# Optimization experiments

Measured on AMD Instinct MI355X. Metric: run time of the kernel, lower is better.

Reference implementation:

```python
import jax, jax.numpy as jnp
import numpy as np

B, N_IMG, D = 256, 128, 768
E, S, H = 3, 44, 1024  # S = ceil(128/3) rounded up to multiple of 4; H = 4*D//E
MAX_SLOTS = 88
LN_EPS = 1e-5


def setup_inputs() -> dict:
    key = jax.random.key(0)
    ks = jax.random.split(key, 12)
    x = jax.random.normal(ks[0], (B, N_IMG + 1, D), dtype=jnp.float32)
    attn_weight = jax.random.uniform(ks[1], (B, N_IMG), dtype=jnp.float32)
    ln_gamma = jnp.ones((D,), jnp.float32)
    ln_beta = jnp.zeros((D,), jnp.float32)
    vsg_w = jax.random.normal(ks[2], (D + 1, D), jnp.float32) / np.sqrt(D + 1)
    vsg_b = jnp.zeros((D,), jnp.float32)
    mu = jax.random.normal(ks[3], (E, D, MAX_SLOTS), jnp.float32) / np.sqrt(D)
    scale = jnp.ones((1,), jnp.float32)
    # per-expert MLP: kaiming-ish / xavier-ish random params
    w1 = jax.random.normal(ks[4], (E, D, H), jnp.float32) * np.sqrt(2.0 / D)
    b1 = jnp.zeros((E, H), jnp.float32)
    w2 = jax.random.normal(ks[5], (E, H, D), jnp.float32) * np.sqrt(2.0 / (H + D))
    b2 = jnp.zeros((E, D), jnp.float32)
    cw1 = jax.random.normal(ks[6], (D, 4 * D), jnp.float32) * np.sqrt(2.0 / D)
    cb1 = jnp.zeros((4 * D,), jnp.float32)
    cw2 = jax.random.normal(ks[7], (4 * D, D), jnp.float32) * np.sqrt(2.0 / (4 * D))
    cb2 = jnp.zeros((D,), jnp.float32)
    return dict(x=x, attn_weight=attn_weight, ln_gamma=ln_gamma, ln_beta=ln_beta,
                vsg_w=vsg_w, vsg_b=vsg_b, mu=mu, scale=scale,
                w1=w1, b1=b1, w2=w2, b2=b2, cw1=cw1, cb1=cb1, cw2=cw2, cb2=cb2)


def reference(x, attn_weight, ln_gamma, ln_beta, vsg_w, vsg_b, mu, scale,
              w1, b1, w2, b2, cw1, cb1, cw2, cb2):
    b, np1, d = x.shape
    n = np1 - 1
    img = x[:, 1:, :]            # [B, N, D]
    cls = x[:, 0, :]             # [B, D]

    # LayerNorm on image tokens
    mean = img.mean(-1, keepdims=True)
    var = img.var(-1, keepdims=True)  # biased, matches torch LayerNorm
    img_n = (img - mean) * jax.lax.rsqrt(var + LN_EPS) * ln_gamma + ln_beta

    # slot bias from [cls_feat, mean attention] -> visible_slot_gen (mode='original')
    attn_feat = attn_weight.mean(axis=1, keepdims=True)            # [B, 1]
    slot_input = jnp.concatenate([cls, attn_feat], axis=-1)        # [B, D+1]
    slot_bias = slot_input @ vsg_w + vsg_b                         # [B, D]

    # adjusted slot prototypes: mu[:, :, :S].permute(1,0,2) + slot_bias broadcast over (E, S)
    adj_mu = mu[:, :, :S].transpose(1, 0, 2)[None] + slot_bias[:, :, None, None]  # [B, D, E, S]

    logits = jnp.einsum('bnd,bdes->bnes', img_n * scale, adj_mu)   # [B, N, E, S]

    # expert group mask from attention thresholds (groups (1,1,1))
    vis = attn_weight > 0.7
    part = (attn_weight >= 0.3) & (attn_weight <= 0.7)
    occ = attn_weight < 0.3
    emask = jnp.stack([vis, part, occ], axis=-1).astype(logits.dtype)  # [B, N, E]
    logits = logits * emask[:, :, :, None]

    # softmax over tokens (dispatch) and over flattened slots (combine)
    dispatch = jax.nn.softmax(logits, axis=1)                      # [B, N, E, S]
    combine = jax.nn.softmax(logits.reshape(b, n, E * S), axis=-1) # [B, N, E*S]

    slot_in = jnp.einsum('bnd,bnes->besd', img, dispatch)          # [B, E, S, D]

    # batched per-expert MLP (fused grouped GEMM instead of python loop)
    h = jax.nn.gelu(jnp.einsum('besd,edh->besh', slot_in, w1) + b1[:, None, :],
                    approximate=False)
    slot_out = jnp.einsum('besh,ehd->besd', h, w2) + b2[:, None, :]  # [B, E, S, D]

    slot_flat = slot_out.reshape(b, E * S, d)
    img_out = jnp.einsum('bsd,bns->bnd', slot_flat, combine)       # [B, N, D]

    # CLS token through its dedicated dense MLP
    cls_h = jax.nn.gelu(cls @ cw1 + cb1, approximate=False)
    cls_out = cls_h @ cw2 + cb2                                    # [B, D]

    return jnp.concatenate([cls_out[:, None, :], img_out], axis=1)  # [B, N+1, D]
```

## Files before the change

kernel.cpp:

```cpp
#include <hip/hip_runtime.h>
#include <hip/hip_bf16.h>
#include <math.h>

#define NB   256
#define NIMG 128
#define DIM  768
#define NE   3
#define NS   44
#define NH   1024
#define ESL  132
#define NTOK (NB*NIMG)
#define MAXSLOTS 88
#define BIGI (1 << 30)

typedef __bf16 bf16x8 __attribute__((ext_vector_type(8)));
typedef float f32x4 __attribute__((ext_vector_type(4)));
typedef unsigned short us8 __attribute__((ext_vector_type(8)));

__device__ __forceinline__ float gelu_f(float v) {
    return 0.5f * v * (1.0f + erff(v * 0.70710678118654752f));
}

__device__ __forceinline__ float block_reduce_sum256(float v, float* red) {
    int tid = threadIdx.x;
    red[tid] = v;
    __syncthreads();
    for (int s = 128; s > 0; s >>= 1) {
        if (tid < s) red[tid] += red[tid + s];
        __syncthreads();
    }
    float r = red[0];
    __syncthreads();
    return r;
}

__global__ void repack_mu_k(const float* __restrict__ mu, __hip_bfloat16* __restrict__ bt) {
    int idx = blockIdx.x * 256 + threadIdx.x;
    if (idx >= 256 * DIM) return;
    int r = idx / DIM, d = idx - r * DIM;
    float v = 0.f;
    if (r < ESL) {
        int e = r / NS, s = r - e * NS;
        v = mu[((size_t)e * DIM + d) * MAXSLOTS + s];
    }
    bt[idx] = __float2bfloat16(v);
}

__global__ void transpose_bf16_k(const float* __restrict__ in, __hip_bfloat16* __restrict__ outp,
                                 int R, int Cc) {
    __shared__ float t[32][33];
    in   += (size_t)blockIdx.z * R * Cc;
    outp += (size_t)blockIdx.z * R * Cc;
    int c0 = blockIdx.x * 32, r0 = blockIdx.y * 32;
    int tx = threadIdx.x, ty = threadIdx.y;
    for (int i = 0; i < 32; i += 8) {
        int r = r0 + ty + i, c = c0 + tx;
        t[ty + i][tx] = (r < R && c < Cc) ? in[(size_t)r * Cc + c] : 0.f;
    }
    __syncthreads();
    for (int i = 0; i < 32; i += 8) {
        int r = c0 + ty + i, c = r0 + tx;
        if (r < Cc && c < R) outp[(size_t)r * R + c] = __float2bfloat16(t[tx][ty + i]);
    }
}

__global__ void cls_bf16_k(const float* __restrict__ x, __hip_bfloat16* __restrict__ cls16) {
    int idx = blockIdx.x * 256 + threadIdx.x;
    if (idx >= NB * DIM) return;
    int b = idx / DIM, j = idx - b * DIM;
    cls16[idx] = __float2bfloat16(x[(size_t)b * 129 * DIM + j]);
}

__global__ void slot_bias_k(const float* __restrict__ x, const float* __restrict__ aw,
                            const float* __restrict__ vsg_w, const float* __restrict__ vsg_b,
                            float* __restrict__ slot_bias) {
    __shared__ float red[256];
    __shared__ float cls[DIM];
    int b = blockIdx.x, tid = threadIdx.x;
    float a = (tid < NIMG) ? aw[b * NIMG + tid] : 0.f;
    float af = block_reduce_sum256(a, red) * (1.0f / NIMG);
    for (int j = tid; j < DIM; j += 256) cls[j] = x[(size_t)b * 129 * DIM + j];
    __syncthreads();
    int j0 = tid, j1 = tid + 256, j2 = tid + 512;
    float acc0 = 0.f, acc1 = 0.f, acc2 = 0.f;
    for (int d = 0; d < DIM; ++d) {
        float c = cls[d];
        const float* wr = vsg_w + (size_t)d * DIM;
        acc0 = fmaf(c, wr[j0], acc0);
        acc1 = fmaf(c, wr[j1], acc1);
        acc2 = fmaf(c, wr[j2], acc2);
    }
    const float* wl = vsg_w + (size_t)DIM * DIM;
    float* out = slot_bias + (size_t)b * DIM;
    out[j0] = acc0 + vsg_b[j0] + af * wl[j0];
    out[j1] = acc1 + vsg_b[j1] + af * wl[j1];
    out[j2] = acc2 + vsg_b[j2] + af * wl[j2];
}

__global__ void ln_t2_k(const float* __restrict__ x, const float* __restrict__ gamma,
                        const float* __restrict__ beta, const float* __restrict__ slot_bias,
                        __hip_bfloat16* __restrict__ img_n, float* __restrict__ t2) {
    __shared__ float red[256];
    int tok = blockIdx.x;
    int b = tok >> 7, n = tok & 127;
    int tid = threadIdx.x;
    const float* row = x + ((size_t)b * 129 + 1 + n) * DIM;
    float v0 = row[tid], v1 = row[tid + 256], v2 = row[tid + 512];
    float s  = block_reduce_sum256(v0 + v1 + v2, red);
    float ss = block_reduce_sum256(v0*v0 + v1*v1 + v2*v2, red);
    float mean = s * (1.0f / DIM);
    float var  = ss * (1.0f / DIM) - mean * mean;
    float inv  = rsqrtf(var + 1e-5f);
    const float* sb = slot_bias + (size_t)b * DIM;
    __hip_bfloat16* orow = img_n + (size_t)tok * DIM;
    float tacc = 0.f;
    int j = tid;
    float y0 = (v0 - mean) * inv * gamma[j] + beta[j]; orow[j] = __float2bfloat16(y0); tacc = fmaf(y0, sb[j], tacc);
    j = tid + 256;
    float y1 = (v1 - mean) * inv * gamma[j] + beta[j]; orow[j] = __float2bfloat16(y1); tacc = fmaf(y1, sb[j], tacc);
    j = tid + 512;
    float y2 = (v2 - mean) * inv * gamma[j] + beta[j]; orow[j] = __float2bfloat16(y2); tacc = fmaf(y2, sb[j], tacc);
    float t = block_reduce_sum256(tacc, red);
    if (tid == 0) t2[tok] = t;
}

__global__ void mask_k(float* __restrict__ L, const float* __restrict__ t2,
                       const float* __restrict__ aw, const float* __restrict__ scale) {
    int idx = blockIdx.x * 256 + threadIdx.x;
    if (idx >= NTOK * ESL) return;
    int tok = idx / ESL, r = idx - tok * ESL;
    int e = r / NS;
    float a = aw[tok];
    int sel = (a > 0.7f) ? 0 : ((a >= 0.3f) ? 1 : 2);
    float v = 0.f;
    if (e == sel) v = scale[0] * (L[idx] + t2[tok]);
    L[idx] = v;
}

__global__ void dispatch_k(const float* __restrict__ L, float* __restrict__ dT) {
    __shared__ float red[128];
    int es = blockIdx.x, b = blockIdx.y, tid = threadIdx.x;
    float v = L[((size_t)(b * NIMG + tid)) * ESL + es];
    red[tid] = v; __syncthreads();
    for (int s = 64; s > 0; s >>= 1) { if (tid < s) red[tid] = fmaxf(red[tid], red[tid + s]); __syncthreads(); }
    float mx = red[0]; __syncthreads();
    float e = __expf(v - mx);
    red[tid] = e; __syncthreads();
    for (int s = 64; s > 0; s >>= 1) { if (tid < s) red[tid] += red[tid + s]; __syncthreads(); }
    float sum = red[0];
    dT[((size_t)b * ESL + es) * NIMG + tid] = e / sum;
}

__global__ void combine_k(const float* __restrict__ L, float* __restrict__ C) {
    int tok = blockIdx.x, lane = threadIdx.x;
    const float* row = L + (size_t)tok * ESL;
    float v0 = row[lane], v1 = row[lane + 64];
    bool has2 = lane < (ESL - 128);
    float v2 = has2 ? row[lane + 128] : -1e30f;
    float m = fmaxf(fmaxf(v0, v1), v2);
    for (int o = 32; o > 0; o >>= 1) m = fmaxf(m, __shfl_xor(m, o));
    float e0 = __expf(v0 - m), e1 = __expf(v1 - m);
    float e2 = has2 ? __expf(v2 - m) : 0.f;
    float s = e0 + e1 + e2;
    for (int o = 32; o > 0; o >>= 1) s += __shfl_xor(s, o);
    float inv = 1.0f / s;
    float* orow = C + (size_t)tok * ESL;
    orow[lane] = e0 * inv;
    orow[lane + 64] = e1 * inv;
    if (has2) orow[lane + 128] = e2 * inv;
}

#define LDSS 40

__global__ __launch_bounds__(256)
void mfma_gemm_k(const __hip_bfloat16* __restrict__ A_, long long aBS, int lda,
                 const __hip_bfloat16* __restrict__ Bt_, long long bBS, int ldb,
                 const float* __restrict__ bias, long long biasBS,
                 void* __restrict__ Cv, long long cBS, int ldc, int cSub, int cOuter,
                 int Nlim, int K, int act, int out_bf16)
{
    const unsigned short* A  = (const unsigned short*)A_  + (long long)blockIdx.z * aBS;
    const unsigned short* Bt = (const unsigned short*)Bt_ + (long long)blockIdx.z * bBS;
    if (bias) bias += (long long)blockIdx.z * biasBS;
    long long cbase = (long long)blockIdx.z * cBS;

    __shared__ unsigned short As[128 * LDSS];
    __shared__ unsigned short Bs[128 * LDSS];

    int tid = threadIdx.x;
    int m0 = blockIdx.y * 128, n0 = blockIdx.x * 128;

    int srow = tid >> 2, sk = (tid & 3) * 8;
    const unsigned short* gA = A  + (long long)(m0 + srow) * lda + sk;
    const unsigned short* gB = Bt + (long long)(n0 + srow) * ldb + sk;
    int lofs  = srow * LDSS + sk;
    int lofs2 = (srow + 64) * LDSS + sk;

    int lane = tid & 63, wv = tid >> 6;
    int wm = (wv >> 1) * 64, wn = (wv & 1) * 64;
    int lrow = lane & 15, quad = lane >> 4;

    int a_off[4], b_off[4];
#pragma unroll
    for (int i = 0; i < 4; ++i) {
        a_off[i] = (wm + i * 16 + lrow) * LDSS + quad * 8;
        b_off[i] = (wn + i * 16 + lrow) * LDSS + quad * 8;
    }

    f32x4 acc[4][4] = {};

    for (int k0 = 0; k0 < K; k0 += 32) {
        us8 a0 = *(const us8*)(gA + k0);
        us8 a1 = *(const us8*)(gA + (long long)64 * lda + k0);
        us8 b0 = *(const us8*)(gB + k0);
        us8 b1 = *(const us8*)(gB + (long long)64 * ldb + k0);
        __syncthreads();
        *(us8*)(As + lofs)  = a0;
        *(us8*)(As + lofs2) = a1;
        *(us8*)(Bs + lofs)  = b0;
        *(us8*)(Bs + lofs2) = b1;
        __syncthreads();
        bf16x8 af[4], bfr[4];
#pragma unroll
        for (int i = 0; i < 4; ++i) {
            af[i]  = *(const bf16x8*)(As + a_off[i]);
            bfr[i] = *(const bf16x8*)(Bs + b_off[i]);
        }
#pragma unroll
        for (int i = 0; i < 4; ++i)
#pragma unroll
            for (int j = 0; j < 4; ++j)
                acc[i][j] = __builtin_amdgcn_mfma_f32_16x16x32_bf16(af[i], bfr[j], acc[i][j], 0, 0, 0);
    }

    float* Cf = (float*)Cv;
    __hip_bfloat16* Cb = (__hip_bfloat16*)Cv;
#pragma unroll
    for (int mi = 0; mi < 4; ++mi) {
#pragma unroll
        for (int r = 0; r < 4; ++r) {
            int row = m0 + wm + mi * 16 + quad * 4 + r;
            int q = row / cSub;
            long long rbase = cbase + (long long)(q * cOuter + (row - q * cSub)) * ldc;
#pragma unroll
            for (int ni = 0; ni < 4; ++ni) {
                int col = n0 + wn + ni * 16 + lrow;
                if (col < Nlim) {
                    float v = acc[mi][ni][r];
                    if (bias) v += bias[col];
                    if (act == 1) v = gelu_f(v);
                    if (out_bf16) Cb[rbase + col] = __float2bfloat16(v);
                    else          Cf[rbase + col] = v;
                }
            }
        }
    }
}

#define GTM 64
#define GTN 64
#define GTK 16

__global__ __launch_bounds__(256)
void gemm_k(const float* __restrict__ A, long long aBS, int lda, int aSub, int aOuter,
            const float* __restrict__ W, long long wBS, int ldw,
            const float* __restrict__ bias, long long biasBS,
            void* __restrict__ Cv, long long cBS, int ldc, int cSub, int cOuter,
            int M, int N, int K, int act, int out_bf16) {
    A += (long long)blockIdx.z * aBS;
    W += (long long)blockIdx.z * wBS;
    if (bias != nullptr) bias += (long long)blockIdx.z * biasBS;
    long long cbase = (long long)blockIdx.z * cBS;

    __shared__ float As[GTK][GTM + 4];
    __shared__ float Ws[GTK][GTN];

    int tid = threadIdx.x;
    int tx = tid & 15, ty = tid >> 4;
    int m0 = blockIdx.y * GTM, n0 = blockIdx.x * GTN;

    int am = tid >> 2, akq = tid & 3;
    int arow_g = m0 + am;
    bool arow_ok = arow_g < M;
    int aq = arow_g / aSub;
    long long aoff = (long long)(aq * aOuter + (arow_g - aq * aSub)) * lda;

    int wn = tid & 63, wg = tid >> 6;
    bool wcol_ok = (n0 + wn) < N;

    float acc[4][4] = {{0.f}};

    for (int k0 = 0; k0 < K; k0 += GTK) {
        float4 av = make_float4(0.f, 0.f, 0.f, 0.f);
        int ak = k0 + akq * 4;
        if (arow_ok && ak < K) av = *(const float4*)(A + aoff + ak);
        As[akq * 4 + 0][am] = av.x;
        As[akq * 4 + 1][am] = av.y;
        As[akq * 4 + 2][am] = av.z;
        As[akq * 4 + 3][am] = av.w;
#pragma unroll
        for (int jj = 0; jj < 4; ++jj) {
            int kk = wg * 4 + jj;
            float wv = 0.f;
            if (wcol_ok && (k0 + kk) < K) wv = W[(long long)(k0 + kk) * ldw + n0 + wn];
            Ws[kk][wn] = wv;
        }
        __syncthreads();
#pragma unroll
        for (int kk = 0; kk < GTK; ++kk) {
            const float4 a4 = *(const float4*)(&As[kk][ty * 4]);
            const float4 w4 = *(const float4*)(&Ws[kk][tx * 4]);
            float a[4] = {a4.x, a4.y, a4.z, a4.w};
            float w[4] = {w4.x, w4.y, w4.z, w4.w};
#pragma unroll
            for (int i = 0; i < 4; ++i)
#pragma unroll
                for (int jq = 0; jq < 4; ++jq)
                    acc[i][jq] = fmaf(a[i], w[jq], acc[i][jq]);
        }
        __syncthreads();
    }

    int col = n0 + tx * 4;
    bool col_ok = col < N;
    float4 bv = make_float4(0.f, 0.f, 0.f, 0.f);
    if (bias != nullptr && col_ok) bv = *(const float4*)(bias + col);
    float* Cf = (float*)Cv;
    __hip_bfloat16* Cb = (__hip_bfloat16*)Cv;
#pragma unroll
    for (int i = 0; i < 4; ++i) {
        int row = m0 + ty * 4 + i;
        if (row < M && col_ok) {
            int q = row / cSub;
            long long coff = cbase + (long long)(q * cOuter + (row - q * cSub)) * ldc + col;
            float4 v = make_float4(acc[i][0] + bv.x, acc[i][1] + bv.y,
                                   acc[i][2] + bv.z, acc[i][3] + bv.w);
            if (act == 1) { v.x = gelu_f(v.x); v.y = gelu_f(v.y); v.z = gelu_f(v.z); v.w = gelu_f(v.w); }
            if (out_bf16) {
                Cb[coff + 0] = __float2bfloat16(v.x);
                Cb[coff + 1] = __float2bfloat16(v.y);
                Cb[coff + 2] = __float2bfloat16(v.z);
                Cb[coff + 3] = __float2bfloat16(v.w);
            } else {
                *(float4*)(Cf + coff) = v;
            }
        }
    }
}

static inline void launch_gemm(hipStream_t st,
                               const float* A, long long aBS, int lda, int aSub, int aOuter,
                               const float* W, long long wBS, int ldw,
                               const float* bias, long long biasBS,
                               void* C, long long cBS, int ldc, int cSub, int cOuter,
                               int M, int N, int K, int act, int batch, int out_bf16) {
    dim3 grid((N + GTN - 1) / GTN, (M + GTM - 1) / GTM, batch);
    gemm_k<<<grid, dim3(256), 0, st>>>(A, aBS, lda, aSub, aOuter, W, wBS, ldw,
                                       bias, biasBS, C, cBS, ldc, cSub, cOuter, M, N, K, act, out_bf16);
}

extern "C" void kernel_launch(void* const* d_in, const int* in_sizes, int n_in,
                              void* d_out, int out_size, void* d_ws, size_t ws_size,
                              hipStream_t stream) {
    const float* x     = (const float*)d_in[0];
    const float* aw    = (const float*)d_in[1];
    const float* gamma = (const float*)d_in[2];
    const float* beta  = (const float*)d_in[3];
    const float* vsg_w = (const float*)d_in[4];
    const float* vsg_b = (const float*)d_in[5];
    const float* mu    = (const float*)d_in[6];
    const float* scale = (const float*)d_in[7];
    const float* w1    = (const float*)d_in[8];
    const float* b1    = (const float*)d_in[9];
    const float* w2    = (const float*)d_in[10];
    const float* b2    = (const float*)d_in[11];
    const float* cw1   = (const float*)d_in[12];
    const float* cb1   = (const float*)d_in[13];
    const float* cw2   = (const float*)d_in[14];
    const float* cb2   = (const float*)d_in[15];
    float* out = (float*)d_out;

    float* ws = (float*)d_ws;

    const long long IMGN_FL = (long long)NTOK * DIM / 2;
    const long long LOG_FL  = (long long)NTOK * ESL;
    __hip_bfloat16* img_n = (__hip_bfloat16*)ws;
    float* logits = ws + IMGN_FL;
    float* dT     = ws + IMGN_FL + LOG_FL;
    __hip_bfloat16* h = (__hip_bfloat16*)ws;
    long long o = IMGN_FL + 2 * LOG_FL;
    float* comb = ws + o;                   o += LOG_FL;
    __hip_bfloat16* slot_in = (__hip_bfloat16*)(ws + o); o += (long long)NE * NB * NS * DIM / 2;
    float* slot_out = ws + o;               o += (long long)NB * ESL * DIM;
    __hip_bfloat16* mu_p  = (__hip_bfloat16*)(ws + o); o += 256 * DIM / 2;
    float* slot_bias = ws + o;              o += NB * DIM;
    float* t2        = ws + o;              o += NTOK;
    __hip_bfloat16* w1t  = (__hip_bfloat16*)(ws + o); o += (long long)NE * NH * DIM / 2;
    __hip_bfloat16* w2t  = (__hip_bfloat16*)(ws + o); o += (long long)NE * DIM * NH / 2;
    __hip_bfloat16* cw1t = (__hip_bfloat16*)(ws + o); o += (long long)4 * DIM * DIM / 2;
    __hip_bfloat16* cw2t = (__hip_bfloat16*)(ws + o); o += (long long)4 * DIM * DIM / 2;
    __hip_bfloat16* cls16 = (__hip_bfloat16*)(ws + o); o += NB * DIM / 2;
    __hip_bfloat16* cls_h = (__hip_bfloat16*)(ws + o); o += (long long)NB * 4 * DIM / 2;

    repack_mu_k<<<(256 * DIM + 255) / 256, 256, 0, stream>>>(mu, mu_p);
    transpose_bf16_k<<<dim3(NH / 32, DIM / 32, NE), dim3(32, 8), 0, stream>>>(w1, w1t, DIM, NH);
    transpose_bf16_k<<<dim3(DIM / 32, NH / 32, NE), dim3(32, 8), 0, stream>>>(w2, w2t, NH, DIM);
    transpose_bf16_k<<<dim3(4 * DIM / 32, DIM / 32, 1), dim3(32, 8), 0, stream>>>(cw1, cw1t, DIM, 4 * DIM);
    transpose_bf16_k<<<dim3(DIM / 32, 4 * DIM / 32, 1), dim3(32, 8), 0, stream>>>(cw2, cw2t, 4 * DIM, DIM);
    cls_bf16_k<<<(NB * DIM + 255) / 256, 256, 0, stream>>>(x, cls16);

    slot_bias_k<<<NB, 256, 0, stream>>>(x, aw, vsg_w, vsg_b, slot_bias);
    ln_t2_k<<<NTOK, 256, 0, stream>>>(x, gamma, beta, slot_bias, img_n, t2);

    mfma_gemm_k<<<dim3(2, NTOK / 128, 1), 256, 0, stream>>>(
        img_n, 0, DIM, mu_p, 0, DIM, nullptr, 0,
        logits, 0, ESL, BIGI, 0, ESL, DIM, 0, 0);

    mask_k<<<(NTOK * ESL + 255) / 256, 256, 0, stream>>>(logits, t2, aw, scale);
    dispatch_k<<<dim3(ESL, NB), 128, 0, stream>>>(logits, dT);
    combine_k<<<NTOK, 64, 0, stream>>>(logits, comb);

    launch_gemm(stream, dT, (long long)ESL * NIMG, NIMG, BIGI, 0,
                x + DIM, (long long)129 * DIM, DIM, nullptr, 0,
                slot_in, (long long)NS * DIM, DIM, NS, NB * NS,
                ESL, DIM, NIMG, 0, NB, 1);

    mfma_gemm_k<<<dim3(NH / 128, NB * NS / 128, NE), 256, 0, stream>>>(
        slot_in, (long long)NB * NS * DIM, DIM,
        w1t, (long long)NH * DIM, DIM, b1, NH,
        h, (long long)NB * NS * NH, NH, BIGI, 0, NH, DIM, 1, 1);

    mfma_gemm_k<<<dim3(DIM / 128, NB * NS / 128, NE), 256, 0, stream>>>(
        h, (long long)NB * NS * NH, NH,
        w2t, (long long)DIM * NH, NH, b2, DIM,
        slot_out, (long long)NS * DIM, DIM, NS, ESL, DIM, NH, 0, 0);

    launch_gemm(stream, comb, (long long)NIMG * ESL, ESL, BIGI, 0,
                slot_out, (long long)ESL * DIM, DIM, nullptr, 0,
                out + DIM, (long long)129 * DIM, DIM, BIGI, 0,
                NIMG, DIM, ESL, 0, NB, 0);

    mfma_gemm_k<<<dim3(4 * DIM / 128, NB / 128, 1), 256, 0, stream>>>(
        cls16, 0, DIM, cw1t, 0, DIM, cb1, 0,
        cls_h, 0, 4 * DIM, BIGI, 0, 4 * DIM, DIM, 1, 1);
    mfma_gemm_k<<<dim3(DIM / 128, NB / 128, 1), 256, 0, stream>>>(
        cls_h, 0, 4 * DIM, cw2t, 0, 4 * DIM, cb2, 0,
        out, 0, DIM, 1, 129, DIM, 4 * DIM, 0, 0);
}
```

Before: 1.077 ms.

## Move dispatch and combine GEMMs to bf16 MFMA with direct-to-LDS loads

The two fp32 SIMT GEMMs (dispatch-weighted token aggregation and combine-weighted slot scatter) are replaced by the bf16 MFMA kernel. To feed it, the dispatch and combine weights are written as bf16, the image tokens are transposed into a bf16 buffer, and the second expert GEMM writes its output transposed with K padded to 160. The MFMA kernel now stages tiles with global_load_lds into an XOR-swizzled LDS layout in place of register staging with padding, and clamps out-of-range rows. This adds a transpose pass over x, lowers the precision of the routing weights and the image input, and the zero padding of slot_outT's extra K columns is not obviously guaranteed.

```diff
diff --git a/kernel.cpp b/kernel.cpp
--- a/kernel.cpp
+++ b/kernel.cpp
@@ -12,10 +12,12 @@
 #define NTOK (NB*NIMG)
 #define MAXSLOTS 88
 #define BIGI (1 << 30)
+#define KPAD 160
 
 typedef __bf16 bf16x8 __attribute__((ext_vector_type(8)));
 typedef float f32x4 __attribute__((ext_vector_type(4)));
-typedef unsigned short us8 __attribute__((ext_vector_type(8)));
+typedef const __attribute__((address_space(1))) void* gas_t;
+typedef __attribute__((address_space(3))) void* las_t;
 
 __device__ __forceinline__ float gelu_f(float v) {
     return 0.5f * v * (1.0f + erff(v * 0.70710678118654752f));
@@ -47,10 +49,10 @@
 }
 
 __global__ void transpose_bf16_k(const float* __restrict__ in, __hip_bfloat16* __restrict__ outp,
-                                 int R, int Cc) {
+                                 int R, int Cc, long long inBS, long long outBS) {
     __shared__ float t[32][33];
-    in   += (size_t)blockIdx.z * R * Cc;
-    outp += (size_t)blockIdx.z * R * Cc;
+    in   += (long long)blockIdx.z * inBS;
+    outp += (long long)blockIdx.z * outBS;
     int c0 = blockIdx.x * 32, r0 = blockIdx.y * 32;
     int tx = threadIdx.x, ty = threadIdx.y;
     for (int i = 0; i < 32; i += 8) {
@@ -137,7 +139,7 @@
     L[idx] = v;
 }
 
-__global__ void dispatch_k(const float* __restrict__ L, float* __restrict__ dT) {
+__global__ void dispatch_k(const float* __restrict__ L, __hip_bfloat16* __restrict__ dT16) {
     __shared__ float red[128];
     int es = blockIdx.x, b = blockIdx.y, tid = threadIdx.x;
     float v = L[((size_t)(b * NIMG + tid)) * ESL + es];
@@ -148,10 +150,10 @@
     red[tid] = e; __syncthreads();
     for (int s = 64; s > 0; s >>= 1) { if (tid < s) red[tid] += red[tid + s]; __syncthreads(); }
     float sum = red[0];
-    dT[((size_t)b * ESL + es) * NIMG + tid] = e / sum;
-}
-
-__global__ void combine_k(const float* __restrict__ L, float* __restrict__ C) {
+    dT16[((size_t)b * ESL + es) * NIMG + tid] = __float2bfloat16(e / sum);
+}
+
+__global__ void combine_k(const float* __restrict__ L, __hip_bfloat16* __restrict__ C) {
     int tok = blockIdx.x, lane = threadIdx.x;
     const float* row = L + (size_t)tok * ESL;
     float v0 = row[lane], v1 = row[lane + 64];
@@ -164,67 +166,74 @@
     float s = e0 + e1 + e2;
     for (int o = 32; o > 0; o >>= 1) s += __shfl_xor(s, o);
     float inv = 1.0f / s;
-    float* orow = C + (size_t)tok * ESL;
-    orow[lane] = e0 * inv;
-    orow[lane + 64] = e1 * inv;
-    if (has2) orow[lane + 128] = e2 * inv;
-}
-
-#define LDSS 40
+    __hip_bfloat16* orow = C + (size_t)tok * KPAD;
+    orow[lane] = __float2bfloat16(e0 * inv);
+    orow[lane + 64] = __float2bfloat16(e1 * inv);
+    if (has2) orow[lane + 128] = __float2bfloat16(e2 * inv);
+    else if (lane < KPAD - 128) orow[lane + 128] = __float2bfloat16(0.f);
+}
 
 __global__ __launch_bounds__(256)
-void mfma_gemm_k(const __hip_bfloat16* __restrict__ A_, long long aBS, int lda,
-                 const __hip_bfloat16* __restrict__ Bt_, long long bBS, int ldb,
-                 const float* __restrict__ bias, long long biasBS,
-                 void* __restrict__ Cv, long long cBS, int ldc, int cSub, int cOuter,
-                 int Nlim, int K, int act, int out_bf16)
+void mfma2_k(const __hip_bfloat16* __restrict__ A_, long long aBS, int lda, int Mrows,
+             const __hip_bfloat16* __restrict__ Bt_, long long bBS, int ldb, int Nrows,
+             const float* __restrict__ bias, long long biasBS,
+             void* __restrict__ Cv, long long cBS, int ldc, int cSub, long long cOuter,
+             int Mlim, int Nlim, int K, int act, int out_bf16, int ctrans)
 {
     const unsigned short* A  = (const unsigned short*)A_  + (long long)blockIdx.z * aBS;
     const unsigned short* Bt = (const unsigned short*)Bt_ + (long long)blockIdx.z * bBS;
     if (bias) bias += (long long)blockIdx.z * biasBS;
     long long cbase = (long long)blockIdx.z * cBS;
 
-    __shared__ unsigned short As[128 * LDSS];
-    __shared__ unsigned short Bs[128 * LDSS];
+    __shared__ unsigned short As[128 * 32];
+    __shared__ unsigned short Bs[128 * 32];
 
     int tid = threadIdx.x;
+    int lane = tid & 63, wv = tid >> 6;
     int m0 = blockIdx.y * 128, n0 = blockIdx.x * 128;
 
-    int srow = tid >> 2, sk = (tid & 3) * 8;
-    const unsigned short* gA = A  + (long long)(m0 + srow) * lda + sk;
-    const unsigned short* gB = Bt + (long long)(n0 + srow) * ldb + sk;
-    int lofs  = srow * LDSS + sk;
-    int lofs2 = (srow + 64) * LDSS + sk;
-
-    int lane = tid & 63, wv = tid >> 6;
+    const unsigned short* ga[2];
+    const unsigned short* gb[2];
+    int ldsoff[2];
+#pragma unroll
+    for (int i = 0; i < 2; ++i) {
+        int j = wv * 2 + i;
+        int p = j * 64 + lane;
+        int r = p >> 2;
+        int cg = (p & 3) ^ ((r >> 1) & 3);
+        int ra = m0 + r; if (ra > Mrows - 1) ra = Mrows - 1;
+        int rb = n0 + r; if (rb > Nrows - 1) rb = Nrows - 1;
+        ga[i] = A  + (long long)ra * lda + cg * 8;
+        gb[i] = Bt + (long long)rb * ldb + cg * 8;
+        ldsoff[i] = j * 512;
+    }
+
+    int lrow = lane & 15, quad = lane >> 4;
     int wm = (wv >> 1) * 64, wn = (wv & 1) * 64;
-    int lrow = lane & 15, quad = lane >> 4;
-
-    int a_off[4], b_off[4];
+    int offA[4], offB[4];
 #pragma unroll
     for (int i = 0; i < 4; ++i) {
-        a_off[i] = (wm + i * 16 + lrow) * LDSS + quad * 8;
-        b_off[i] = (wn + i * 16 + lrow) * LDSS + quad * 8;
+        int rowa = wm + i * 16 + lrow;
+        offA[i] = rowa * 32 + ((quad ^ ((rowa >> 1) & 3)) * 8);
+        int rowb = wn + i * 16 + lrow;
+        offB[i] = rowb * 32 + ((quad ^ ((rowb >> 1) & 3)) * 8);
     }
 
     f32x4 acc[4][4] = {};
 
     for (int k0 = 0; k0 < K; k0 += 32) {
-        us8 a0 = *(const us8*)(gA + k0);
-        us8 a1 = *(const us8*)(gA + (long long)64 * lda + k0);
-        us8 b0 = *(const us8*)(gB + k0);
-        us8 b1 = *(const us8*)(gB + (long long)64 * ldb + k0);
         __syncthreads();
-        *(us8*)(As + lofs)  = a0;
-        *(us8*)(As + lofs2) = a1;
-        *(us8*)(Bs + lofs)  = b0;
-        *(us8*)(Bs + lofs2) = b1;
+#pragma unroll
+        for (int i = 0; i < 2; ++i) {
+            __builtin_amdgcn_global_load_lds((gas_t)(ga[i] + k0), (las_t)(As + ldsoff[i]), 16, 0, 0);
+            __builtin_amdgcn_global_load_lds((gas_t)(gb[i] + k0), (las_t)(Bs + ldsoff[i]), 16, 0, 0);
+        }
         __syncthreads();
         bf16x8 af[4], bfr[4];
 #pragma unroll
         for (int i = 0; i < 4; ++i) {
-            af[i]  = *(const bf16x8*)(As + a_off[i]);
-            bfr[i] = *(const bf16x8*)(Bs + b_off[i]);
+            af[i]  = *(const bf16x8*)(As + offA[i]);
+            bfr[i] = *(const bf16x8*)(Bs + offB[i]);
         }
 #pragma unroll
         for (int i = 0; i < 4; ++i)
@@ -240,8 +249,11 @@
 #pragma unroll
         for (int r = 0; r < 4; ++r) {
             int row = m0 + wm + mi * 16 + quad * 4 + r;
+            if (row >= Mlim) continue;
             int q = row / cSub;
-            long long rbase = cbase + (long long)(q * cOuter + (row - q * cSub)) * ldc;
+            int sl = row - q * cSub;
+            long long rb = ctrans ? (cbase + (long long)q * cOuter + sl)
+                                  : (cbase + ((long long)q * cOuter + sl) * ldc);
 #pragma unroll
             for (int ni = 0; ni < 4; ++ni) {
                 int col = n0 + wn + ni * 16 + lrow;
@@ -249,114 +261,25 @@
                     float v = acc[mi][ni][r];
                     if (bias) v += bias[col];
                     if (act == 1) v = gelu_f(v);
-                    if (out_bf16) Cb[rbase + col] = __float2bfloat16(v);
-                    else          Cf[rbase + col] = v;
+                    long long off = ctrans ? (rb + (long long)col * ldc) : (rb + col);
+                    if (out_bf16) Cb[off] = __float2bfloat16(v);
+                    else          Cf[off] = v;
                 }
             }
         }
     }
 }
 
-#define GTM 64
-#define GTN 64
-#define GTK 16
-
-__global__ __launch_bounds__(256)
-void gemm_k(const float* __restrict__ A, long long aBS, int lda, int aSub, int aOuter,
-            const float* __restrict__ W, long long wBS, int ldw,
-            const float* __restrict__ bias, long long biasBS,
-            void* __restrict__ Cv, long long cBS, int ldc, int cSub, int cOuter,
-            int M, int N, int K, int act, int out_bf16) {
-    A += (long long)blockIdx.z * aBS;
-    W += (long long)blockIdx.z * wBS;
-    if (bias != nullptr) bias += (long long)blockIdx.z * biasBS;
-    long long cbase = (long long)blockIdx.z * cBS;
-
-    __shared__ float As[GTK][GTM + 4];
-    __shared__ float Ws[GTK][GTN];
-
-    int tid = threadIdx.x;
-    int tx = tid & 15, ty = tid >> 4;
-    int m0 = blockIdx.y * GTM, n0 = blockIdx.x * GTN;
-
-    int am = tid >> 2, akq = tid & 3;
-    int arow_g = m0 + am;
-    bool arow_ok = arow_g < M;
-    int aq = arow_g / aSub;
-    long long aoff = (long long)(aq * aOuter + (arow_g - aq * aSub)) * lda;
-
-    int wn = tid & 63, wg = tid >> 6;
-    bool wcol_ok = (n0 + wn) < N;
-
-    float acc[4][4] = {{0.f}};
-
-    for (int k0 = 0; k0 < K; k0 += GTK) {
-        float4 av = make_float4(0.f, 0.f, 0.f, 0.f);
-        int ak = k0 + akq * 4;
-        if (arow_ok && ak < K) av = *(const float4*)(A + aoff + ak);
-        As[akq * 4 + 0][am] = av.x;
-        As[akq * 4 + 1][am] = av.y;
-        As[akq * 4 + 2][am] = av.z;
-        As[akq * 4 + 3][am] = av.w;
-#pragma unroll
-        for (int jj = 0; jj < 4; ++jj) {
-            int kk = wg * 4 + jj;
-            float wv = 0.f;
-            if (wcol_ok && (k0 + kk) < K) wv = W[(long long)(k0 + kk) * ldw + n0 + wn];
-            Ws[kk][wn] = wv;
-        }
-        __syncthreads();
-#pragma unroll
-        for (int kk = 0; kk < GTK; ++kk) {
-            const float4 a4 = *(const float4*)(&As[kk][ty * 4]);
-            const float4 w4 = *(const float4*)(&Ws[kk][tx * 4]);
-            float a[4] = {a4.x, a4.y, a4.z, a4.w};
-            float w[4] = {w4.x, w4.y, w4.z, w4.w};
-#pragma unroll
-            for (int i = 0; i < 4; ++i)
-#pragma unroll
-                for (int jq = 0; jq < 4; ++jq)
-                    acc[i][jq] = fmaf(a[i], w[jq], acc[i][jq]);
-        }
-        __syncthreads();
-    }
-
-    int col = n0 + tx * 4;
-    bool col_ok = col < N;
-    float4 bv = make_float4(0.f, 0.f, 0.f, 0.f);
-    if (bias != nullptr && col_ok) bv = *(const float4*)(bias + col);
-    float* Cf = (float*)Cv;
-    __hip_bfloat16* Cb = (__hip_bfloat16*)Cv;
-#pragma unroll
-    for (int i = 0; i < 4; ++i) {
-        int row = m0 + ty * 4 + i;
-        if (row < M && col_ok) {
-            int q = row / cSub;
-            long long coff = cbase + (long long)(q * cOuter + (row - q * cSub)) * ldc + col;
-            float4 v = make_float4(acc[i][0] + bv.x, acc[i][1] + bv.y,
-                                   acc[i][2] + bv.z, acc[i][3] + bv.w);
-            if (act == 1) { v.x = gelu_f(v.x); v.y = gelu_f(v.y); v.z = gelu_f(v.z); v.w = gelu_f(v.w); }
-            if (out_bf16) {
-                Cb[coff + 0] = __float2bfloat16(v.x);
-                Cb[coff + 1] = __float2bfloat16(v.y);
-                Cb[coff + 2] = __float2bfloat16(v.z);
-                Cb[coff + 3] = __float2bfloat16(v.w);
-            } else {
-                *(float4*)(Cf + coff) = v;
-            }
-        }
-    }
-}
-
-static inline void launch_gemm(hipStream_t st,
-                               const float* A, long long aBS, int lda, int aSub, int aOuter,
-                               const float* W, long long wBS, int ldw,
-                               const float* bias, long long biasBS,
-                               void* C, long long cBS, int ldc, int cSub, int cOuter,
-                               int M, int N, int K, int act, int batch, int out_bf16) {
-    dim3 grid((N + GTN - 1) / GTN, (M + GTM - 1) / GTM, batch);
-    gemm_k<<<grid, dim3(256), 0, st>>>(A, aBS, lda, aSub, aOuter, W, wBS, ldw,
-                                       bias, biasBS, C, cBS, ldc, cSub, cOuter, M, N, K, act, out_bf16);
+static inline void mfma2(hipStream_t st, dim3 grid,
+                         const void* A, long long aBS, int lda, int Mrows,
+                         const void* Bt, long long bBS, int ldb, int Nrows,
+                         const float* bias, long long biasBS,
+                         void* C, long long cBS, int ldc, int cSub, long long cOuter,
+                         int Mlim, int Nlim, int K, int act, int obf, int ct) {
+    mfma2_k<<<grid, dim3(256), 0, st>>>((const __hip_bfloat16*)A, aBS, lda, Mrows,
+                                        (const __hip_bfloat16*)Bt, bBS, ldb, Nrows,
+                                        bias, biasBS, C, cBS, ldc, cSub, cOuter,
+                                        Mlim, Nlim, K, act, obf, ct);
 }
 
 extern "C" void kernel_launch(void* const* d_in, const int* in_sizes, int n_in,
@@ -384,66 +307,73 @@
 
     const long long IMGN_FL = (long long)NTOK * DIM / 2;
     const long long LOG_FL  = (long long)NTOK * ESL;
+    const long long REG1_FL = (long long)NE * NB * NS * NH / 2;
     __hip_bfloat16* img_n = (__hip_bfloat16*)ws;
     float* logits = ws + IMGN_FL;
-    float* dT     = ws + IMGN_FL + LOG_FL;
     __hip_bfloat16* h = (__hip_bfloat16*)ws;
-    long long o = IMGN_FL + 2 * LOG_FL;
-    float* comb = ws + o;                   o += LOG_FL;
+    long long o = REG1_FL;
+    __hip_bfloat16* dT16    = (__hip_bfloat16*)(ws + o); o += (long long)NB * ESL * NIMG / 2;
+    __hip_bfloat16* comb_p  = (__hip_bfloat16*)(ws + o); o += (long long)NTOK * KPAD / 2;
+    __hip_bfloat16* imgT    = (__hip_bfloat16*)(ws + o);
+    __hip_bfloat16* slot_outT = imgT;                    o += (long long)NB * DIM * KPAD / 2;
     __hip_bfloat16* slot_in = (__hip_bfloat16*)(ws + o); o += (long long)NE * NB * NS * DIM / 2;
-    float* slot_out = ws + o;               o += (long long)NB * ESL * DIM;
-    __hip_bfloat16* mu_p  = (__hip_bfloat16*)(ws + o); o += 256 * DIM / 2;
-    float* slot_bias = ws + o;              o += NB * DIM;
-    float* t2        = ws + o;              o += NTOK;
-    __hip_bfloat16* w1t  = (__hip_bfloat16*)(ws + o); o += (long long)NE * NH * DIM / 2;
-    __hip_bfloat16* w2t  = (__hip_bfloat16*)(ws + o); o += (long long)NE * DIM * NH / 2;
-    __hip_bfloat16* cw1t = (__hip_bfloat16*)(ws + o); o += (long long)4 * DIM * DIM / 2;
-    __hip_bfloat16* cw2t = (__hip_bfloat16*)(ws + o); o += (long long)4 * DIM * DIM / 2;
-    __hip_bfloat16* cls16 = (__hip_bfloat16*)(ws + o); o += NB * DIM / 2;
-    __hip_bfloat16* cls_h = (__hip_bfloat16*)(ws + o); o += (long long)NB * 4 * DIM / 2;
+    __hip_bfloat16* mu_p    = (__hip_bfloat16*)(ws + o); o += 256 * DIM / 2;
+    float* slot_bias = ws + o;                           o += NB * DIM;
+    float* t2        = ws + o;                           o += NTOK;
+    __hip_bfloat16* w1t  = (__hip_bfloat16*)(ws + o);    o += (long long)NE * NH * DIM / 2;
+    __hip_bfloat16* w2t  = (__hip_bfloat16*)(ws + o);    o += (long long)NE * DIM * NH / 2;
+    __hip_bfloat16* cw1t = (__hip_bfloat16*)(ws + o);    o += (long long)4 * DIM * DIM / 2;
+    __hip_bfloat16* cw2t = (__hip_bfloat16*)(ws + o);    o += (long long)4 * DIM * DIM / 2;
+    __hip_bfloat16* cls16 = (__hip_bfloat16*)(ws + o);   o += NB * DIM / 2;
+    __hip_bfloat16* cls_h = (__hip_bfloat16*)(ws + o);   o += (long long)NB * 4 * DIM / 2;
 
     repack_mu_k<<<(256 * DIM + 255) / 256, 256, 0, stream>>>(mu, mu_p);
-    transpose_bf16_k<<<dim3(NH / 32, DIM / 32, NE), dim3(32, 8), 0, stream>>>(w1, w1t, DIM, NH);
-    transpose_bf16_k<<<dim3(DIM / 32, NH / 32, NE), dim3(32, 8), 0, stream>>>(w2, w2t, NH, DIM);
-    transpose_bf16_k<<<dim3(4 * DIM / 32, DIM / 32, 1), dim3(32, 8), 0, stream>>>(cw1, cw1t, DIM, 4 * DIM);
-    transpose_bf16_k<<<dim3(DIM / 32, 4 * DIM / 32, 1), dim3(32, 8), 0, stream>>>(cw2, cw2t, 4 * DIM, DIM);
+    transpose_bf16_k<<<dim3(NH / 32, DIM / 32, NE), dim3(32, 8), 0, stream>>>(w1, w1t, DIM, NH, (long long)DIM * NH, (long long)NH * DIM);
+    transpose_bf16_k<<<dim3(DIM / 32, NH / 32, NE), dim3(32, 8), 0, stream>>>(w2, w2t, NH, DIM, (long long)NH * DIM, (long long)DIM * NH);
+    transpose_bf16_k<<<dim3(4 * DIM / 32, DIM / 32, 1), dim3(32, 8), 0, stream>>>(cw1, cw1t, DIM, 4 * DIM, 0, 0);
+    transpose_bf16_k<<<dim3(DIM / 32, 4 * DIM / 32, 1), dim3(32, 8), 0, stream>>>(cw2, cw2t, 4 * DIM, DIM, 0, 0);
     cls_bf16_k<<<(NB * DIM + 255) / 256, 256, 0, stream>>>(x, cls16);
+    transpose_bf16_k<<<dim3(DIM / 32, NIMG / 32, NB), dim3(32, 8), 0, stream>>>(x + DIM, imgT, NIMG, DIM, (long long)129 * DIM, (long long)DIM * NIMG);
 
     slot_bias_k<<<NB, 256, 0, stream>>>(x, aw, vsg_w, vsg_b, slot_bias);
     ln_t2_k<<<NTOK, 256, 0, stream>>>(x, gamma, beta, slot_bias, img_n, t2);
 
-    mfma_gemm_k<<<dim3(2, NTOK / 128, 1), 256, 0, stream>>>(
-        img_n, 0, DIM, mu_p, 0, DIM, nullptr, 0,
-        logits, 0, ESL, BIGI, 0, ESL, DIM, 0, 0);
+    mfma2(stream, dim3(2, NTOK / 128, 1),
+          img_n, 0, DIM, NTOK, mu_p, 0, DIM, 256, nullptr, 0,
+          logits, 0, ESL, BIGI, 0, NTOK, ESL, DIM, 0, 0, 0);
 
     mask_k<<<(NTOK * ESL + 255) / 256, 256, 0, stream>>>(logits, t2, aw, scale);
-    dispatch_k<<<dim3(ESL, NB), 128, 0, stream>>>(logits, dT);
-    combine_k<<<NTOK, 64, 0, stream>>>(logits, comb);
-
-    launch_gemm(stream, dT, (long long)ESL * NIMG, NIMG, BIGI, 0,
-                x + DIM, (long long)129 * DIM, DIM, nullptr, 0,
-                slot_in, (long long)NS * DIM, DIM, NS, NB * NS,
-                ESL, DIM, NIMG, 0, NB, 1);
-
-    mfma_gemm_k<<<dim3(NH / 128, NB * NS / 128, NE), 256, 0, stream>>>(
-        slot_in, (long long)NB * NS * DIM, DIM,
-        w1t, (long long)NH * DIM, DIM, b1, NH,
-        h, (long long)NB * NS * NH, NH, BIGI, 0, NH, DIM, 1, 1);
-
-    mfma_gemm_k<<<dim3(DIM / 128, NB * NS / 128, NE), 256, 0, stream>>>(
-        h, (long long)NB * NS * NH, NH,
-        w2t, (long long)DIM * NH, NH, b2, DIM,
-        slot_out, (long long)NS * DIM, DIM, NS, ESL, DIM, NH, 0, 0);
-
-    launch_gemm(stream, comb, (long long)NIMG * ESL, ESL, BIGI, 0,
-                slot_out, (long long)ESL * DIM, DIM, nullptr, 0,
-                out + DIM, (long long)129 * DIM, DIM, BIGI, 0,
-                NIMG, DIM, ESL, 0, NB, 0);
-
-    mfma_gemm_k<<<dim3(4 * DIM / 128, NB / 128, 1), 256, 0, stream>>>(
-        cls16, 0, DIM, cw1t, 0, DIM, cb1, 0,
-        cls_h, 0, 4 * DIM, BIGI, 0, 4 * DIM, DIM, 1, 1);
-    mfma_gemm_k<<<dim3(DIM / 128, NB / 128, 1), 256, 0, stream>>>(
-        cls_h, 0, 4 * DIM, cw2t, 0, 4 * DIM, cb2, 0,
-        out, 0, DIM, 1, 129, DIM, 4 * DIM, 0, 0);
-}
+    dispatch_k<<<dim3(ESL, NB), 128, 0, stream>>>(logits, dT16);
+    combine_k<<<NTOK, 64, 0, stream>>>(logits, comb_p);
+
+    mfma2(stream, dim3(DIM / 128, 2, NB),
+          dT16, (long long)ESL * NIMG, NIMG, ESL,
+          imgT, (long long)DIM * NIMG, NIMG, DIM, nullptr, 0,
+          slot_in, (long long)NS * DIM, DIM, NS, NB * NS,
+          ESL, DIM, NIMG, 0, 1, 0);
+
+    mfma2(stream, dim3(NH / 128, NB * NS / 128, NE),
+          slot_in, (long long)NB * NS * DIM, DIM, NB * NS,
+          w1t, (long long)NH * DIM, DIM, NH, b1, NH,
+          h, (long long)NB * NS * NH, NH, BIGI, 0,
+          NB * NS, NH, DIM, 1, 1, 0);
+
+    mfma2(stream, dim3(DIM / 128, NB * NS / 128, NE),
+          h, (long long)NB * NS * NH, NH, NB * NS,
+          w2t, (long long)DIM * NH, NH, DIM, b2, DIM,
+          slot_outT, NS, KPAD, NS, (long long)DIM * KPAD,
+          NB * NS, DIM, NH, 0, 1, 1);
+
+    mfma2(stream, dim3(DIM / 128, 1, NB),
+          comb_p, (long long)NIMG * KPAD, KPAD, NIMG,
+          slot_outT, (long long)DIM * KPAD, KPAD, DIM, nullptr, 0,
+          out + DIM, (long long)129 * DIM, DIM, BIGI, 0,
+          NIMG, DIM, KPAD, 0, 0, 0);
+
+    mfma2(stream, dim3(4 * DIM / 128, NB / 128, 1),
+          cls16, 0, DIM, NB, cw1t, 0, DIM, 4 * DIM, cb1, 0,
+          cls_h, 0, 4 * DIM, BIGI, 0, NB, 4 * DIM, DIM, 1, 1, 0);
+    mfma2(stream, dim3(DIM / 128, NB / 128, 1),
+          cls_h, 0, 4 * DIM, NB, cw2t, 0, 4 * DIM, DIM, cb2, 0,
+          out, 0, DIM, 1, 129, NB, DIM, 4 * DIM, 0, 0, 0);
+}
```

Measured after the change: 1.055 ms. -2.0%, faster.
